# Optimization experiments

Hardware: AMD Instinct MI355X
Metric: run time of the kernel (lower is better)

Reference implementation:

```python
import jax, jax.numpy as jnp
import numpy as np

TEMP = 0.5  # matches temperature init kwarg
EPS = 1e-12  # F.normalize eps


def _l2norm(x):
    # F.normalize(x, dim=1): x / max(||x||, eps)
    n = jnp.linalg.norm(x, axis=1, keepdims=True)
    return x / jnp.maximum(n, EPS)


def setup_inputs() -> dict:
    key = jax.random.key(0)
    k1, k2 = jax.random.split(key)
    B, D = 4096, 256
    return {
        "x_i": jax.random.normal(k1, (B, D), dtype=jnp.float32),
        "x_j": jax.random.normal(k2, (B, D), dtype=jnp.float32),
    }


def reference(x_i, x_j):
    B = x_i.shape[0]
    z = jnp.concatenate([_l2norm(x_i), _l2norm(x_j)], axis=0)  # [2B, D]
    # cosine similarity of normalized rows == matmul (avoids NxNxD broadcast)
    sim = (z @ z.T) / TEMP  # [2B, 2B]
    idx = jnp.arange(B)
    # diagonals at offsets +B and -B = positive pairs
    pos = jnp.concatenate([sim[idx, idx + B], sim[idx + B, idx]])  # [2B]
    exp_sim = jnp.exp(sim)
    # neg = all off-diagonal entries per row (neg_mask = ~eye(2B))
    exp_neg = exp_sim.sum(axis=1) - jnp.exp(jnp.diagonal(sim))  # [2B]
    exp_pos = jnp.exp(pos)
    loss = -jnp.log(exp_pos / (exp_pos + exp_neg))
    return loss.mean()
```

## Files before the change

### kernel.cpp

```cpp
#include <hip/hip_runtime.h>
#include <hip/hip_bf16.h>

typedef __attribute__((ext_vector_type(8))) short bf16x8;
typedef __attribute__((ext_vector_type(4))) float f32x4;
typedef __attribute__((ext_vector_type(8))) unsigned short ushort8;
typedef __attribute__((ext_vector_type(4))) unsigned short ushort4v;

constexpr int BB = 4096;
constexpr int D  = 256;
constexpr int R2 = 8192;
constexpr int NSPLIT = 8;
constexpr float SQRT2 = 1.41421356237309515f;
constexpr float E2 = 7.38905609893065f;

__device__ __forceinline__ unsigned short f2bf(float f) {
    __hip_bfloat16 h = __float2bfloat16(f);
    return *reinterpret_cast<unsigned short*>(&h);
}

__global__ __launch_bounds__(256) void norm_kernel(const float* __restrict__ xi,
                                                   const float* __restrict__ xj,
                                                   unsigned short* __restrict__ z,
                                                   float* __restrict__ pos) {
    const int wid = threadIdx.x >> 6, lane = threadIdx.x & 63;
    const int k = blockIdx.x * 4 + wid;
    const float4* a4 = reinterpret_cast<const float4*>(xi + (size_t)k * D);
    const float4* b4 = reinterpret_cast<const float4*>(xj + (size_t)k * D);
    float4 a = a4[lane], b = b4[lane];
    float ssi = a.x*a.x + a.y*a.y + a.z*a.z + a.w*a.w;
    float ssj = b.x*b.x + b.y*b.y + b.z*b.z + b.w*b.w;
    float dot = a.x*b.x + a.y*b.y + a.z*b.z + a.w*b.w;
#pragma unroll
    for (int off = 32; off; off >>= 1) {
        ssi += __shfl_xor(ssi, off);
        ssj += __shfl_xor(ssj, off);
        dot += __shfl_xor(dot, off);
    }
    const float inv_i = 1.0f / fmaxf(sqrtf(ssi), 1e-12f);
    const float inv_j = 1.0f / fmaxf(sqrtf(ssj), 1e-12f);
    const float si = inv_i * SQRT2, sj = inv_j * SQRT2;
    ushort4v zi = { f2bf(a.x*si), f2bf(a.y*si), f2bf(a.z*si), f2bf(a.w*si) };
    ushort4v zj = { f2bf(b.x*sj), f2bf(b.y*sj), f2bf(b.z*sj), f2bf(b.w*sj) };
    *reinterpret_cast<ushort4v*>(z + (size_t)k * D + lane*4)        = zi;
    *reinterpret_cast<ushort4v*>(z + (size_t)(k+BB) * D + lane*4)   = zj;
    if (lane == 0) pos[k] = dot * inv_i * inv_j * 2.0f;
}

__global__ __launch_bounds__(256) void sim_kernel(const unsigned short* __restrict__ z,
                                                  float* __restrict__ partial) {
    __shared__ unsigned short tb[64][D + 8];
    const int wid = threadIdx.x >> 6, lane = threadIdx.x & 63;
    const int lrow = lane & 15, quad = lane >> 4;
    const int r0 = blockIdx.x * 128 + wid * 32;

    bf16x8 afrag[2][8];
#pragma unroll
    for (int m = 0; m < 2; ++m)
#pragma unroll
        for (int kk = 0; kk < 8; ++kk)
            afrag[m][kk] = *reinterpret_cast<const bf16x8*>(
                z + (size_t)(r0 + m*16 + lrow) * D + kk*32 + quad*8);

    float racc[2][4] = {{0.f,0.f,0.f,0.f},{0.f,0.f,0.f,0.f}};
    const int cbase = blockIdx.y * (R2 / NSPLIT);

    for (int ct = 0; ct < (R2 / NSPLIT) / 64; ++ct) {
        const int c0 = cbase + ct * 64;
        __syncthreads();
#pragma unroll
        for (int i = 0; i < 8; ++i) {
            const int chunk = threadIdx.x + 256 * i;
            const int cr = chunk >> 5, ck = chunk & 31;
            *reinterpret_cast<ushort8*>(&tb[cr][ck*8]) =
                *reinterpret_cast<const ushort8*>(z + (size_t)(c0 + cr) * D + ck*8);
        }
        __syncthreads();
#pragma unroll
        for (int n = 0; n < 4; ++n) {
            bf16x8 bfrag[8];
#pragma unroll
            for (int kk = 0; kk < 8; ++kk)
                bfrag[kk] = *reinterpret_cast<const bf16x8*>(&tb[n*16 + lrow][kk*32 + quad*8]);
#pragma unroll
            for (int m = 0; m < 2; ++m) {
                f32x4 c = {0.f, 0.f, 0.f, 0.f};
#pragma unroll
                for (int kk = 0; kk < 8; ++kk)
                    c = __builtin_amdgcn_mfma_f32_16x16x32_bf16(afrag[m][kk], bfrag[kk], c, 0, 0, 0);
#pragma unroll
                for (int j = 0; j < 4; ++j)
                    racc[m][j] += __expf(c[j]);
            }
        }
    }

#pragma unroll
    for (int m = 0; m < 2; ++m)
#pragma unroll
        for (int j = 0; j < 4; ++j) {
            float v = racc[m][j];
            v += __shfl_xor(v, 1);
            v += __shfl_xor(v, 2);
            v += __shfl_xor(v, 4);
            v += __shfl_xor(v, 8);
            if (lrow == 0)
                partial[(size_t)blockIdx.y * R2 + r0 + m*16 + quad*4 + j] = v;
        }
}

__global__ __launch_bounds__(1024) void finalize_kernel(const float* __restrict__ partial,
                                                        const float* __restrict__ pos,
                                                        float* __restrict__ out) {
    __shared__ float wsum[16];
    const int tid = threadIdx.x;
    float lsum = 0.f;
    for (int r = tid; r < R2; r += 1024) {
        float S = 0.f;
#pragma unroll
        for (int s = 0; s < NSPLIT; ++s) S += partial[(size_t)s * R2 + r];
        const float p = pos[r & (BB - 1)];
        lsum += __logf(__expf(p) + S - E2) - p;
    }
#pragma unroll
    for (int off = 32; off; off >>= 1) lsum += __shfl_xor(lsum, off);
    if ((tid & 63) == 0) wsum[tid >> 6] = lsum;
    __syncthreads();
    if (tid == 0) {
        float t = 0.f;
#pragma unroll
        for (int i = 0; i < 16; ++i) t += wsum[i];
        out[0] = t / (float)R2;
    }
}

extern "C" void kernel_launch(void* const* d_in, const int* in_sizes, int n_in,
                              void* d_out, int out_size, void* d_ws, size_t ws_size,
                              hipStream_t stream) {
    (void)in_sizes; (void)n_in; (void)out_size; (void)ws_size;
    const float* xi = (const float*)d_in[0];
    const float* xj = (const float*)d_in[1];
    float* out = (float*)d_out;

    unsigned short* z = (unsigned short*)d_ws;
    float* partial = (float*)((char*)d_ws + (size_t)R2 * D * 2);
    float* pos     = (float*)((char*)d_ws + (size_t)R2 * D * 2 + NSPLIT*R2*4);

    norm_kernel<<<BB / 4, 256, 0, stream>>>(xi, xj, z, pos);
    sim_kernel<<<dim3(R2 / 128, NSPLIT), 256, 0, stream>>>(z, partial);
    finalize_kernel<<<1, 1024, 0, stream>>>(partial, pos, out);
}
```

Before: 102.7 us.

## Double-buffer B tiles with register prefetch, XOR-swizzle LDS, grow per-wave rows

```diff
diff --git a/kernel.cpp b/kernel.cpp
--- a/kernel.cpp
+++ b/kernel.cpp
@@ -9,7 +9,9 @@
 constexpr int BB = 4096;
 constexpr int D  = 256;
 constexpr int R2 = 8192;
-constexpr int NSPLIT = 8;
+constexpr int NSPLIT = 16;
+constexpr int CT = 64;
+constexpr int NT = (R2 / NSPLIT) / CT;
 constexpr float SQRT2 = 1.41421356237309515f;
 constexpr float E2 = 7.38905609893065f;
 
@@ -46,43 +48,66 @@
     if (lane == 0) pos[k] = dot * inv_i * inv_j * 2.0f;
 }
 
-__global__ __launch_bounds__(256) void sim_kernel(const unsigned short* __restrict__ z,
-                                                  float* __restrict__ partial) {
-    __shared__ unsigned short tb[64][D + 8];
-    const int wid = threadIdx.x >> 6, lane = threadIdx.x & 63;
+__global__ __launch_bounds__(256, 2) void sim_kernel(const unsigned short* __restrict__ z,
+                                                     float* __restrict__ partial) {
+    __shared__ unsigned short tb[2][CT * D];
+    const int tid = threadIdx.x;
+    const int wid = tid >> 6, lane = tid & 63;
     const int lrow = lane & 15, quad = lane >> 4;
-    const int r0 = blockIdx.x * 128 + wid * 32;
+    const int r0 = blockIdx.x * 256 + wid * 64;
+    const int cbase = blockIdx.y * (R2 / NSPLIT);
 
-    bf16x8 afrag[2][8];
+    bf16x8 afrag[4][8];
 #pragma unroll
-    for (int m = 0; m < 2; ++m)
+    for (int m = 0; m < 4; ++m)
 #pragma unroll
         for (int kk = 0; kk < 8; ++kk)
             afrag[m][kk] = *reinterpret_cast<const bf16x8*>(
                 z + (size_t)(r0 + m*16 + lrow) * D + kk*32 + quad*8);
 
-    float racc[2][4] = {{0.f,0.f,0.f,0.f},{0.f,0.f,0.f,0.f}};
-    const int cbase = blockIdx.y * (R2 / NSPLIT);
+    float racc[4][4];
+#pragma unroll
+    for (int m = 0; m < 4; ++m)
+#pragma unroll
+        for (int j = 0; j < 4; ++j) racc[m][j] = 0.f;
 
-    for (int ct = 0; ct < (R2 / NSPLIT) / 64; ++ct) {
-        const int c0 = cbase + ct * 64;
-        __syncthreads();
+    ushort8 sreg[8];
+#pragma unroll
+    for (int i = 0; i < 8; ++i) {
+        const int L = i * 256 + tid;
+        const int r = L >> 5, cl = L & 31;
+        sreg[i] = *reinterpret_cast<const ushort8*>(z + (size_t)(cbase + r) * D + cl*8);
+    }
+
+    for (int ct = 0; ct < NT; ++ct) {
+        const int buf = ct & 1;
 #pragma unroll
         for (int i = 0; i < 8; ++i) {
-            const int chunk = threadIdx.x + 256 * i;
-            const int cr = chunk >> 5, ck = chunk & 31;
-            *reinterpret_cast<ushort8*>(&tb[cr][ck*8]) =
-                *reinterpret_cast<const ushort8*>(z + (size_t)(c0 + cr) * D + ck*8);
+            const int L = i * 256 + tid;
+            const int r = L >> 5, cl = L & 31;
+            *reinterpret_cast<ushort8*>(&tb[buf][r * D + (cl ^ (r & 7)) * 8]) = sreg[i];
         }
         __syncthreads();
+        if (ct + 1 < NT) {
+            const int c0n = cbase + (ct + 1) * CT;
+#pragma unroll
+            for (int i = 0; i < 8; ++i) {
+                const int L = i * 256 + tid;
+                const int r = L >> 5, cl = L & 31;
+                sreg[i] = *reinterpret_cast<const ushort8*>(z + (size_t)(c0n + r) * D + cl*8);
+            }
+        }
 #pragma unroll
         for (int n = 0; n < 4; ++n) {
             bf16x8 bfrag[8];
 #pragma unroll
-            for (int kk = 0; kk < 8; ++kk)
-                bfrag[kk] = *reinterpret_cast<const bf16x8*>(&tb[n*16 + lrow][kk*32 + quad*8]);
+            for (int kk = 0; kk < 8; ++kk) {
+                const int r = n*16 + lrow;
+                const int cp = (kk*4 + quad) ^ (lrow & 7);
+                bfrag[kk] = *reinterpret_cast<const bf16x8*>(&tb[buf][r * D + cp * 8]);
+            }
 #pragma unroll
-            for (int m = 0; m < 2; ++m) {
+            for (int m = 0; m < 4; ++m) {
                 f32x4 c = {0.f, 0.f, 0.f, 0.f};
 #pragma unroll
                 for (int kk = 0; kk < 8; ++kk)
@@ -92,10 +117,11 @@
                     racc[m][j] += __expf(c[j]);
             }
         }
+        __syncthreads();
     }
 
 #pragma unroll
-    for (int m = 0; m < 2; ++m)
+    for (int m = 0; m < 4; ++m)
 #pragma unroll
         for (int j = 0; j < 4; ++j) {
             float v = racc[m][j];
@@ -146,6 +172,6 @@
     float* pos     = (float*)((char*)d_ws + (size_t)R2 * D * 2 + NSPLIT*R2*4);
 
     norm_kernel<<<BB / 4, 256, 0, stream>>>(xi, xj, z, pos);
-    sim_kernel<<<dim3(R2 / 128, NSPLIT), 256, 0, stream>>>(z, partial);
+    sim_kernel<<<dim3(R2 / 256, NSPLIT), 256, 0, stream>>>(z, partial);
     finalize_kernel<<<1, 1024, 0, stream>>>(partial, pos, out);
 }
```

Result: slower. 123.7 us (+20.4%).
